# Optimization experiments

Hardware: AMD Instinct MI355X
Metric: run time of the kernel (lower is better)

The kernel has to match this reference:

```python
import jax, jax.numpy as jnp
import numpy as np

N = 100000
E = 1600000
D_IN = 128
D_OUT = 128
EPS_GIN = 0.0  # GIN epsilon from __init__
LN_EPS = 1e-5
PROJ_EPS = 1e-9


def setup_inputs() -> dict:
    key = jax.random.key(0)
    ks = jax.random.split(key, 9)
    x = jax.random.normal(ks[0], (N, D_IN), dtype=jnp.float32)
    edge_index = jax.random.randint(ks[1], (2, E), 0, N, dtype=jnp.int64)
    edge_weight = jax.random.normal(ks[2], (E,), dtype=jnp.float32)
    # MLP params (Linear(in,out) -> ReLU -> Linear(out,out)), torch default-ish init
    s1 = 1.0 / np.sqrt(D_IN)
    s2 = 1.0 / np.sqrt(D_OUT)
    W1 = jax.random.uniform(ks[3], (D_IN, D_OUT), jnp.float32, -s1, s1)
    b1 = jax.random.uniform(ks[4], (D_OUT,), jnp.float32, -s1, s1)
    W2 = jax.random.uniform(ks[5], (D_OUT, D_OUT), jnp.float32, -s2, s2)
    b2 = jax.random.uniform(ks[6], (D_OUT,), jnp.float32, -s2, s2)
    gamma = jnp.ones((D_OUT,), jnp.float32)
    beta = jnp.zeros((D_OUT,), jnp.float32)
    return {"x": x, "edge_index": edge_index, "edge_weight": edge_weight,
            "W1": W1, "b1": b1, "W2": W2, "b2": b2, "gamma": gamma, "beta": beta}


def _aggregate(x, edge_index, edge_weight):
    # Per-target-node softmax over edge weights, then weighted projective average.
    src = edge_index[0]
    tgt = edge_index[1]
    n = x.shape[0]
    m = jax.ops.segment_max(edge_weight, tgt, num_segments=n)          # [N]
    ew = jnp.exp(edge_weight - m[tgt])                                  # [E], stable softmax numerator
    denom = jax.ops.segment_sum(ew, tgt, num_segments=n)               # [N]
    w = ew / denom[tgt]                                                 # [E], per-node softmax weights
    msg = w[:, None] * x[src]                                           # [E, D]
    agg = jax.ops.segment_sum(msg, tgt, num_segments=n)                # [N, D] weighted sum
    # projective_average: normalize the weighted combination to the unit sphere
    norm = jnp.linalg.norm(agg, axis=-1, keepdims=True)
    return agg / (norm + PROJ_EPS)                                      # zero rows stay zero


def _layer_norm(h, gamma, beta):
    mu = jnp.mean(h, axis=-1, keepdims=True)
    var = jnp.var(h, axis=-1, keepdims=True)
    return gamma * (h - mu) * jax.lax.rsqrt(var + LN_EPS) + beta


def reference(x, edge_index, edge_weight, W1, b1, W2, b2, gamma, beta):
    neigh = _aggregate(x, edge_index, edge_weight)
    combined = (1.0 + EPS_GIN) * x + neigh
    h = jnp.maximum(combined @ W1 + b1, 0.0)
    h = h @ W2 + b2
    h = _layer_norm(h, gamma, beta)
    # dropout: eval mode -> identity
    return h
```

## Files before the change

### kernel.cpp

```cpp
#include <hip/hip_runtime.h>
#include <hip/hip_bf16.h>

#define D 128
#define CH 2048
#define BSH 9
#define SLAB 9216

typedef __attribute__((ext_vector_type(8))) short short8;
typedef __attribute__((ext_vector_type(4))) float f32x4;
typedef __attribute__((ext_vector_type(4))) int int4v;
typedef __attribute__((ext_vector_type(2))) int int2v;
typedef __attribute__((ext_vector_type(4))) float float4v;
typedef __attribute__((ext_vector_type(2))) float float2v;
typedef __attribute__((ext_vector_type(4))) unsigned uint4v;
typedef __attribute__((ext_vector_type(2))) unsigned uint2v;
typedef _Float16 half2_t __attribute__((ext_vector_type(2)));

__device__ __forceinline__ unsigned short us_bf16(float f) {
    return __bfloat16_as_ushort(__float2bfloat16(f));
}
__device__ __forceinline__ unsigned pack_bf16(float a, float b) {
    return (unsigned)us_bf16(a) | ((unsigned)us_bf16(b) << 16);
}
__device__ __forceinline__ unsigned pack_f16(float a, float b) {
    unsigned short ua = __builtin_bit_cast(unsigned short, (_Float16)a);
    unsigned short ub = __builtin_bit_cast(unsigned short, (_Float16)b);
    return (unsigned)ua | ((unsigned)ub << 16);
}
__device__ __forceinline__ float f16_lo(int y) {
    return (float)__builtin_bit_cast(_Float16, (unsigned short)(y & 0xffff));
}
__device__ __forceinline__ half2_t as_h2(unsigned u) {
    return __builtin_bit_cast(half2_t, u);
}
__device__ __forceinline__ int2v nt_load2(const int2* p) {
    return __builtin_nontemporal_load(reinterpret_cast<const int2v*>(p));
}

__global__ __launch_bounds__(256) void k_prep(const float* __restrict__ x,
                                              unsigned* __restrict__ xh,
                                              unsigned* __restrict__ xq, int nf4,
                                              const float* __restrict__ W1,
                                              const float* __restrict__ W2,
                                              unsigned short* __restrict__ W1t,
                                              unsigned short* __restrict__ W2t) {
    int i0 = blockIdx.x * blockDim.x + threadIdx.x;
    int stride = gridDim.x * blockDim.x;
    const float4v* x4 = reinterpret_cast<const float4v*>(x);
    uint2v* xh2 = reinterpret_cast<uint2v*>(xh);
    for (int i = i0; i < nf4; i += stride) {
        float4v v = x4[i];
        uint2v o;
        o.x = pack_f16(v.x, v.y);
        o.y = pack_f16(v.z, v.w);
        xh2[i] = o;
        int p = __builtin_amdgcn_cvt_pk_fp8_f32(v.x, v.y, 0, false);
        p = __builtin_amdgcn_cvt_pk_fp8_f32(v.z, v.w, p, true);
        xq[i] = (unsigned)p;
    }
    if (i0 < 16384) {
        int k = i0 >> 7, nn = i0 & 127;
        W1t[nn * 128 + k] = us_bf16(W1[i0]);
        W2t[nn * 128 + k] = us_bf16(W2[i0]);
    }
}

__global__ __launch_bounds__(256) void k_binA(
    const int* __restrict__ src, const int* __restrict__ tgt,
    const float* __restrict__ ew, int* __restrict__ bcnt,
    int2* __restrict__ stage, int E, int nbuk)
{
    __shared__ int2 recs[CH];
    __shared__ unsigned short bslot[CH];
    __shared__ int sh[256];
    __shared__ int lbase[256];
    __shared__ int gofs[256];

    int tid = threadIdx.x;
    int c0 = blockIdx.x * CH;
    int chunkCnt = min(CH, E - c0);

    sh[tid] = 0;
    __syncthreads();

    int myb[8], mypos[8], mysrc[8]; unsigned myy[8];
    #pragma unroll
    for (int k = 0; k < 8; ++k) {
        int idx = k * 256 + tid;
        myb[k] = -1;
        if (idx < chunkCnt) {
            int e = c0 + idx;
            int t = __builtin_nontemporal_load(&tgt[e]);
            int b = t >> BSH;
            float expw = __expf(__builtin_nontemporal_load(&ew[e]));
            unsigned short h = __builtin_bit_cast(unsigned short, (_Float16)expw);
            myb[k] = b;
            myy[k] = ((unsigned)(t & ((1 << BSH) - 1)) << 16) | (unsigned)h;
            mysrc[k] = __builtin_nontemporal_load(&src[e]);
            mypos[k] = atomicAdd(&sh[b], 1);
        }
    }
    __syncthreads();
    int cnt_b = sh[tid];
    for (int off = 1; off < 256; off <<= 1) {
        int o = (tid >= off) ? sh[tid - off] : 0;
        __syncthreads();
        sh[tid] += o;
        __syncthreads();
    }
    int lb = sh[tid] - cnt_b;
    lbase[tid] = lb;
    if (cnt_b > 0 && tid < nbuk) {
        int gb = atomicAdd(&bcnt[tid], cnt_b) + tid * SLAB;
        gofs[tid] = gb - lb;
    }
    __syncthreads();
    #pragma unroll
    for (int k = 0; k < 8; ++k) {
        if (myb[k] >= 0) {
            int slot = lbase[myb[k]] + mypos[k];
            recs[slot] = make_int2(mysrc[k], (int)myy[k]);
            bslot[slot] = (unsigned short)myb[k];
        }
    }
    __syncthreads();
    for (int i = tid; i < chunkCnt; i += 256) {
        int b = bslot[i];
        stage[gofs[b] + i] = recs[i];
    }
}

__global__ __launch_bounds__(256) void k_binB(
    const int* __restrict__ bcnt, const int2* __restrict__ stage,
    int2* __restrict__ csr, int* __restrict__ rowptr, int n)
{
    __shared__ int lcnt[1 << BSH];
    __shared__ float ldenom[1 << BSH];
    __shared__ int sc[256];
    int b = blockIdx.x;
    int tid = threadIdx.x;
    int node0 = b << BSH;
    int nn = min(1 << BSH, n - node0);
    int s0 = b * SLAB;
    int s1 = s0 + bcnt[b];

    for (int j = tid; j < (1 << BSH); j += 256) { lcnt[j] = 0; ldenom[j] = 0.f; }
    __syncthreads();

    for (int i = s0 + tid; i < s1; i += 256) {
        int2v rec = nt_load2(&stage[i]);
        int tl = ((unsigned)rec.y) >> 16;
        _Float16 hw = __builtin_bit_cast(_Float16, (unsigned short)(rec.y & 0xffff));
        atomicAdd(&lcnt[tl], 1);
        atomicAdd(&ldenom[tl], (float)hw);
    }
    __syncthreads();

    for (int j = tid; j < (1 << BSH); j += 256) {
        float d = ldenom[j];
        ldenom[j] = (d > 0.f) ? (1.f / d) : 0.f;
    }
    int v0 = lcnt[2 * tid], v1 = lcnt[2 * tid + 1];
    int tsum = v0 + v1;
    sc[tid] = tsum;
    __syncthreads();
    for (int off = 1; off < 256; off <<= 1) {
        int o = (tid >= off) ? sc[tid - off] : 0;
        __syncthreads();
        sc[tid] += o;
        __syncthreads();
    }
    int excl = sc[tid] - tsum;
    int p0 = s0 + excl, p1 = s0 + excl + v0;
    if (2 * tid < nn)     rowptr[node0 + 2 * tid] = p0;
    if (2 * tid + 1 < nn) rowptr[node0 + 2 * tid + 1] = p1;
    __syncthreads();
    lcnt[2 * tid] = p0;
    lcnt[2 * tid + 1] = p1;
    __syncthreads();

    for (int i = s0 + tid; i < s1; i += 256) {
        int2v rec = nt_load2(&stage[i]);
        int tl = ((unsigned)rec.y) >> 16;
        _Float16 hw = __builtin_bit_cast(_Float16, (unsigned short)(rec.y & 0xffff));
        float wn = (float)hw * ldenom[tl];
        unsigned short wb = __builtin_bit_cast(unsigned short, (_Float16)wn);
        unsigned wp = (unsigned)wb | ((unsigned)wb << 16);
        int pos = atomicAdd(&lcnt[tl], 1);
        csr[pos] = make_int2(rec.x, (int)wp);
    }
}

__global__ __launch_bounds__(256) void k_agg(
    const int* __restrict__ rowptr, const int* __restrict__ bcnt,
    const int2* __restrict__ csr,
    const uint4v* __restrict__ xq4, const uint4v* __restrict__ xh4,
    uint4v* __restrict__ cmb4, int n)
{
    int w = threadIdx.x >> 6;
    int lane = threadIdx.x & 63;
    int node = blockIdx.x * 4 + w;
    if (node >= n) node = n - 1;

    int b = node >> BSH;
    int r0 = rowptr[node];
    int r1;
    if ((((node + 1) & ((1 << BSH) - 1)) == 0) || (node + 1 >= n))
        r1 = b * SLAB + bcnt[b];
    else
        r1 = rowptr[node + 1];
    int cnt = r1 - r0;

    int eg = lane >> 3;
    int dg = lane & 7;

    float a[16];
    #pragma unroll
    for (int j = 0; j < 16; ++j) a[j] = 0.f;

    int last = (cnt > 0) ? cnt - 1 : 0;
    for (int base = 0; base < cnt; base += 32) {
        #pragma unroll
        for (int i = 0; i < 4; ++i) {
            if (base + i * 8 >= cnt) break;
            int e = base + i * 8 + eg;
            bool valid = e < cnt;
            int2v cr = nt_load2(&csr[r0 + (valid ? e : last)]);
            float wn = valid ? f16_lo(cr.y) : 0.f;
            uint4v q = xq4[cr.x * 8 + dg];
            #pragma unroll
            for (int h = 0; h < 4; ++h) {
                int word = (int)((h == 0) ? q.x : (h == 1) ? q.y : (h == 2) ? q.z : q.w);
                float2v flo = __builtin_amdgcn_cvt_pk_f32_fp8(word, false);
                float2v fhi = __builtin_amdgcn_cvt_pk_f32_fp8(word, true);
                a[h * 4 + 0] = fmaf(wn, flo.x, a[h * 4 + 0]);
                a[h * 4 + 1] = fmaf(wn, flo.y, a[h * 4 + 1]);
                a[h * 4 + 2] = fmaf(wn, fhi.x, a[h * 4 + 2]);
                a[h * 4 + 3] = fmaf(wn, fhi.y, a[h * 4 + 3]);
            }
        }
    }

    #pragma unroll
    for (int m = 8; m <= 32; m <<= 1)
        #pragma unroll
        for (int j = 0; j < 16; ++j)
            a[j] += __shfl_xor(a[j], m);

    float ss = 0.f;
    #pragma unroll
    for (int j = 0; j < 16; ++j) ss = fmaf(a[j], a[j], ss);
    #pragma unroll
    for (int m = 1; m <= 4; m <<= 1) ss += __shfl_xor(ss, m);
    float rn = 1.f / (sqrtf(ss) + 1e-9f);

    if (eg == 0) {
        #pragma unroll
        for (int h = 0; h < 2; ++h) {
            uint4v hx = xh4[node * 16 + dg * 2 + h];
            half2_t x0 = as_h2(hx.x), x1 = as_h2(hx.y), x2 = as_h2(hx.z), x3 = as_h2(hx.w);
            const float* ah = &a[h * 8];
            uint4v o;
            o.x = pack_bf16((float)x0.x + ah[0] * rn, (float)x0.y + ah[1] * rn);
            o.y = pack_bf16((float)x1.x + ah[2] * rn, (float)x1.y + ah[3] * rn);
            o.z = pack_bf16((float)x2.x + ah[4] * rn, (float)x2.y + ah[5] * rn);
            o.w = pack_bf16((float)x3.x + ah[6] * rn, (float)x3.y + ah[7] * rn);
            cmb4[node * 16 + dg * 2 + h] = o;
        }
    }
}

__global__ __launch_bounds__(256) void k_mlp(
    const uint4v* __restrict__ cmb4,
    const unsigned short* __restrict__ W1t, const unsigned short* __restrict__ W2t,
    const float* __restrict__ b1, const float* __restrict__ b2,
    const float* __restrict__ gamma, const float* __restrict__ beta,
    float* __restrict__ out, int n)
{
    __shared__ __align__(16) unsigned short sA[64][136];

    int node0 = blockIdx.x * 64;
    int w = threadIdx.x >> 6;
    int lane = threadIdx.x & 63;
    int lr = lane & 15;
    int lg = lane >> 4;
    int mr = w * 16;

    for (int idx = threadIdx.x; idx < 64 * 16; idx += 256) {
        int row = idx >> 4, seg = idx & 15;
        int gr = node0 + row; if (gr >= n) gr = n - 1;
        uint4v v = cmb4[gr * 16 + seg];
        *reinterpret_cast<uint4v*>(&sA[row][seg * 8]) = v;
    }
    __syncthreads();

    short8 aF[4];
    #pragma unroll
    for (int kt = 0; kt < 4; ++kt)
        aF[kt] = *reinterpret_cast<const short8*>(&sA[mr + lr][kt * 32 + lg * 8]);

    #pragma unroll
    for (int nt = 0; nt < 8; ++nt) {
        f32x4 c = {0.f, 0.f, 0.f, 0.f};
        #pragma unroll
        for (int kt = 0; kt < 4; ++kt) {
            short8 bF = *reinterpret_cast<const short8*>(
                &W1t[(nt * 16 + lr) * 128 + kt * 32 + lg * 8]);
            c = __builtin_amdgcn_mfma_f32_16x16x32_bf16(aF[kt], bF, c, 0, 0, 0);
        }
        float b1v = b1[nt * 16 + lr];
        #pragma unroll
        for (int reg = 0; reg < 4; ++reg) {
            float h = fmaxf(c[reg] + b1v, 0.f);
            sA[mr + lg * 4 + reg][nt * 16 + lr] = us_bf16(h);
        }
    }
    __syncthreads();

    short8 a2F[4];
    #pragma unroll
    for (int kt = 0; kt < 4; ++kt)
        a2F[kt] = *reinterpret_cast<const short8*>(&sA[mr + lr][kt * 32 + lg * 8]);

    f32x4 c2[8];
    float b2v[8], gv[8], bev[8];
    #pragma unroll
    for (int nt = 0; nt < 8; ++nt) {
        c2[nt] = (f32x4){0.f, 0.f, 0.f, 0.f};
        #pragma unroll
        for (int kt = 0; kt < 4; ++kt) {
            short8 bF = *reinterpret_cast<const short8*>(
                &W2t[(nt * 16 + lr) * 128 + kt * 32 + lg * 8]);
            c2[nt] = __builtin_amdgcn_mfma_f32_16x16x32_bf16(a2F[kt], bF, c2[nt], 0, 0, 0);
        }
        int col = nt * 16 + lr;
        b2v[nt] = b2[col]; gv[nt] = gamma[col]; bev[nt] = beta[col];
    }

    float rs[4] = {0.f, 0.f, 0.f, 0.f}, sq[4] = {0.f, 0.f, 0.f, 0.f};
    #pragma unroll
    for (int nt = 0; nt < 8; ++nt)
        #pragma unroll
        for (int reg = 0; reg < 4; ++reg) {
            float v = c2[nt][reg] + b2v[nt];
            rs[reg] += v; sq[reg] += v * v;
        }
    #pragma unroll
    for (int off = 1; off <= 8; off <<= 1)
        #pragma unroll
        for (int reg = 0; reg < 4; ++reg) {
            rs[reg] += __shfl_xor(rs[reg], off);
            sq[reg] += __shfl_xor(sq[reg], off);
        }
    float mu[4], rstd[4];
    #pragma unroll
    for (int reg = 0; reg < 4; ++reg) {
        mu[reg] = rs[reg] * (1.f / 128.f);
        float var = sq[reg] * (1.f / 128.f) - mu[reg] * mu[reg];
        rstd[reg] = rsqrtf(var + 1e-5f);
    }

    #pragma unroll
    for (int nt = 0; nt < 8; ++nt)
        #pragma unroll
        for (int reg = 0; reg < 4; ++reg) {
            int gr = node0 + mr + lg * 4 + reg;
            if (gr < n) {
                float v = c2[nt][reg] + b2v[nt];
                out[gr * 128 + nt * 16 + lr] = gv[nt] * (v - mu[reg]) * rstd[reg] + bev[nt];
            }
        }
}

extern "C" void kernel_launch(void* const* d_in, const int* in_sizes, int n_in,
                              void* d_out, int out_size, void* d_ws, size_t ws_size,
                              hipStream_t stream) {
    const float* x     = (const float*)d_in[0];
    const int*   ei    = (const int*)d_in[1];
    const float* ew    = (const float*)d_in[2];
    const float* W1    = (const float*)d_in[3];
    const float* b1    = (const float*)d_in[4];
    const float* W2    = (const float*)d_in[5];
    const float* b2    = (const float*)d_in[6];
    const float* gamma = (const float*)d_in[7];
    const float* beta  = (const float*)d_in[8];

    int n = in_sizes[0] / D;
    int E = in_sizes[2];
    const int* src = ei;
    const int* tgt = ei + E;

    int nbuk = (n + (1 << BSH) - 1) >> BSH;

    char* ws = (char*)d_ws;
    int2*     csr    = (int2*)ws;     ws += (size_t)nbuk * SLAB * sizeof(int2);
    unsigned* xh     = (unsigned*)ws; ws += (size_t)n * 64 * sizeof(unsigned);
    unsigned* xq     = (unsigned*)ws; ws += (size_t)n * 32 * sizeof(unsigned);
    unsigned* cmb    = (unsigned*)ws; ws += (size_t)n * 64 * sizeof(unsigned);
    unsigned short* W1t = (unsigned short*)ws; ws += 128 * 128 * sizeof(unsigned short);
    unsigned short* W2t = (unsigned short*)ws; ws += 128 * 128 * sizeof(unsigned short);
    int*      rowptr = (int*)ws;      ws += ((size_t)n + 1) * sizeof(int);
    int*      bcnt   = (int*)ws;      ws += 256 * sizeof(int);
    int2*     stage  = (int2*)cmb;

    hipMemsetAsync((void*)bcnt, 0, 256 * sizeof(int), stream);

    int nf4 = n * D / 4;
    k_prep<<<2048, 256, 0, stream>>>(x, xh, xq, nf4, W1, W2, W1t, W2t);

    int nchunk = (E + CH - 1) / CH;
    k_binA<<<nchunk, 256, 0, stream>>>(src, tgt, ew, bcnt, stage, E, nbuk);
    k_binB<<<nbuk, 256, 0, stream>>>(bcnt, stage, csr, rowptr, n);

    k_agg<<<(n + 3) / 4, 256, 0, stream>>>(rowptr, bcnt, csr,
                                           (const uint4v*)xq, (const uint4v*)xh,
                                           (uint4v*)cmb, n);

    k_mlp<<<(n + 63) / 64, 256, 0, stream>>>((const uint4v*)cmb, W1t, W2t,
                                             b1, b2, gamma, beta,
                                             (float*)d_out, n);
}
```

Before: 211.2 us.

## Drop softmax denominator, fuse prep into binning, use packed fp16 shuffle reduction

The softmax denominator pass in k_binB is removed and the raw exp weights go straight into the CSR. This relies on the projective normalisation dividing out any positive per-node scale, and it drops one LDS float-atomic pass plus a reciprocal step. The x/W conversion kernel is folded into the binning kernel as extra specialised blocks, saving a launch and letting the two run concurrently. The cross-lane reduction in k_agg now shuffles packed fp16 pairs scaled by 1/256, which halves the shuffle count at some precision and overflow risk.

```diff
diff --git a/kernel.cpp b/kernel.cpp
--- a/kernel.cpp
+++ b/kernel.cpp
@@ -5,6 +5,7 @@
 #define CH 2048
 #define BSH 9
 #define SLAB 9216
+#define PREP_BLK 1024
 
 typedef __attribute__((ext_vector_type(8))) short short8;
 typedef __attribute__((ext_vector_type(4))) float f32x4;
@@ -37,38 +38,14 @@
     return __builtin_nontemporal_load(reinterpret_cast<const int2v*>(p));
 }
 
-__global__ __launch_bounds__(256) void k_prep(const float* __restrict__ x,
-                                              unsigned* __restrict__ xh,
-                                              unsigned* __restrict__ xq, int nf4,
-                                              const float* __restrict__ W1,
-                                              const float* __restrict__ W2,
-                                              unsigned short* __restrict__ W1t,
-                                              unsigned short* __restrict__ W2t) {
-    int i0 = blockIdx.x * blockDim.x + threadIdx.x;
-    int stride = gridDim.x * blockDim.x;
-    const float4v* x4 = reinterpret_cast<const float4v*>(x);
-    uint2v* xh2 = reinterpret_cast<uint2v*>(xh);
-    for (int i = i0; i < nf4; i += stride) {
-        float4v v = x4[i];
-        uint2v o;
-        o.x = pack_f16(v.x, v.y);
-        o.y = pack_f16(v.z, v.w);
-        xh2[i] = o;
-        int p = __builtin_amdgcn_cvt_pk_fp8_f32(v.x, v.y, 0, false);
-        p = __builtin_amdgcn_cvt_pk_fp8_f32(v.z, v.w, p, true);
-        xq[i] = (unsigned)p;
-    }
-    if (i0 < 16384) {
-        int k = i0 >> 7, nn = i0 & 127;
-        W1t[nn * 128 + k] = us_bf16(W1[i0]);
-        W2t[nn * 128 + k] = us_bf16(W2[i0]);
-    }
-}
-
-__global__ __launch_bounds__(256) void k_binA(
+__global__ __launch_bounds__(256) void k_prepbinA(
     const int* __restrict__ src, const int* __restrict__ tgt,
     const float* __restrict__ ew, int* __restrict__ bcnt,
-    int2* __restrict__ stage, int E, int nbuk)
+    int2* __restrict__ stage, int E, int nbuk, int nchunk,
+    const float* __restrict__ x, unsigned* __restrict__ xh,
+    unsigned* __restrict__ xq, int nf4,
+    const float* __restrict__ W1, const float* __restrict__ W2,
+    unsigned short* __restrict__ W1t, unsigned short* __restrict__ W2t)
 {
     __shared__ int2 recs[CH];
     __shared__ unsigned short bslot[CH];
@@ -77,6 +54,31 @@
     __shared__ int gofs[256];
 
     int tid = threadIdx.x;
+
+    if (blockIdx.x >= (unsigned)nchunk) {
+        int pb = blockIdx.x - nchunk;
+        int i0 = pb * 256 + tid;
+        int stride = PREP_BLK * 256;
+        const float4v* x4 = reinterpret_cast<const float4v*>(x);
+        uint2v* xh2 = reinterpret_cast<uint2v*>(xh);
+        for (int i = i0; i < nf4; i += stride) {
+            float4v v = x4[i];
+            uint2v o;
+            o.x = pack_f16(v.x, v.y);
+            o.y = pack_f16(v.z, v.w);
+            xh2[i] = o;
+            int p = __builtin_amdgcn_cvt_pk_fp8_f32(v.x, v.y, 0, false);
+            p = __builtin_amdgcn_cvt_pk_fp8_f32(v.z, v.w, p, true);
+            xq[i] = (unsigned)p;
+        }
+        if (i0 < 16384) {
+            int k = i0 >> 7, nn = i0 & 127;
+            W1t[nn * 128 + k] = us_bf16(W1[i0]);
+            W2t[nn * 128 + k] = us_bf16(W2[i0]);
+        }
+        return;
+    }
+
     int c0 = blockIdx.x * CH;
     int chunkCnt = min(CH, E - c0);
 
@@ -135,7 +137,6 @@
     int2* __restrict__ csr, int* __restrict__ rowptr, int n)
 {
     __shared__ int lcnt[1 << BSH];
-    __shared__ float ldenom[1 << BSH];
     __shared__ int sc[256];
     int b = blockIdx.x;
     int tid = threadIdx.x;
@@ -144,22 +145,15 @@
     int s0 = b * SLAB;
     int s1 = s0 + bcnt[b];
 
-    for (int j = tid; j < (1 << BSH); j += 256) { lcnt[j] = 0; ldenom[j] = 0.f; }
+    for (int j = tid; j < (1 << BSH); j += 256) lcnt[j] = 0;
     __syncthreads();
 
     for (int i = s0 + tid; i < s1; i += 256) {
         int2v rec = nt_load2(&stage[i]);
-        int tl = ((unsigned)rec.y) >> 16;
-        _Float16 hw = __builtin_bit_cast(_Float16, (unsigned short)(rec.y & 0xffff));
-        atomicAdd(&lcnt[tl], 1);
-        atomicAdd(&ldenom[tl], (float)hw);
-    }
-    __syncthreads();
-
-    for (int j = tid; j < (1 << BSH); j += 256) {
-        float d = ldenom[j];
-        ldenom[j] = (d > 0.f) ? (1.f / d) : 0.f;
-    }
+        atomicAdd(&lcnt[((unsigned)rec.y) >> 16], 1);
+    }
+    __syncthreads();
+
     int v0 = lcnt[2 * tid], v1 = lcnt[2 * tid + 1];
     int tsum = v0 + v1;
     sc[tid] = tsum;
@@ -181,13 +175,8 @@
 
     for (int i = s0 + tid; i < s1; i += 256) {
         int2v rec = nt_load2(&stage[i]);
-        int tl = ((unsigned)rec.y) >> 16;
-        _Float16 hw = __builtin_bit_cast(_Float16, (unsigned short)(rec.y & 0xffff));
-        float wn = (float)hw * ldenom[tl];
-        unsigned short wb = __builtin_bit_cast(unsigned short, (_Float16)wn);
-        unsigned wp = (unsigned)wb | ((unsigned)wb << 16);
-        int pos = atomicAdd(&lcnt[tl], 1);
-        csr[pos] = make_int2(rec.x, (int)wp);
+        int pos = atomicAdd(&lcnt[((unsigned)rec.y) >> 16], 1);
+        csr[pos] = make_int2(rec.x, rec.y);
     }
 }
 
@@ -242,14 +231,30 @@
     }
 
     #pragma unroll
+    for (int j = 0; j < 16; ++j) a[j] *= 0.00390625f;
+    unsigned u[8];
+    #pragma unroll
+    for (int j = 0; j < 8; ++j)
+        u[j] = __builtin_bit_cast(unsigned,
+                   __builtin_amdgcn_cvt_pkrtz(a[2 * j], a[2 * j + 1]));
+    #pragma unroll
     for (int m = 8; m <= 32; m <<= 1)
         #pragma unroll
-        for (int j = 0; j < 16; ++j)
-            a[j] += __shfl_xor(a[j], m);
+        for (int j = 0; j < 8; ++j) {
+            half2_t s = as_h2(u[j]) + as_h2((unsigned)__shfl_xor((int)u[j], m));
+            u[j] = __builtin_bit_cast(unsigned, s);
+        }
+    float af[16];
+    #pragma unroll
+    for (int j = 0; j < 8; ++j) {
+        half2_t s = as_h2(u[j]);
+        af[2 * j] = (float)s.x;
+        af[2 * j + 1] = (float)s.y;
+    }
 
     float ss = 0.f;
     #pragma unroll
-    for (int j = 0; j < 16; ++j) ss = fmaf(a[j], a[j], ss);
+    for (int j = 0; j < 16; ++j) ss = fmaf(af[j], af[j], ss);
     #pragma unroll
     for (int m = 1; m <= 4; m <<= 1) ss += __shfl_xor(ss, m);
     float rn = 1.f / (sqrtf(ss) + 1e-9f);
@@ -259,7 +264,7 @@
         for (int h = 0; h < 2; ++h) {
             uint4v hx = xh4[node * 16 + dg * 2 + h];
             half2_t x0 = as_h2(hx.x), x1 = as_h2(hx.y), x2 = as_h2(hx.z), x3 = as_h2(hx.w);
-            const float* ah = &a[h * 8];
+            const float* ah = &af[h * 8];
             uint4v o;
             o.x = pack_bf16((float)x0.x + ah[0] * rn, (float)x0.y + ah[1] * rn);
             o.y = pack_bf16((float)x1.x + ah[2] * rn, (float)x1.y + ah[3] * rn);
@@ -406,10 +411,11 @@
     hipMemsetAsync((void*)bcnt, 0, 256 * sizeof(int), stream);
 
     int nf4 = n * D / 4;
-    k_prep<<<2048, 256, 0, stream>>>(x, xh, xq, nf4, W1, W2, W1t, W2t);
-
     int nchunk = (E + CH - 1) / CH;
-    k_binA<<<nchunk, 256, 0, stream>>>(src, tgt, ew, bcnt, stage, E, nbuk);
+    k_prepbinA<<<nchunk + PREP_BLK, 256, 0, stream>>>(
+        src, tgt, ew, bcnt, stage, E, nbuk, nchunk,
+        x, xh, xq, nf4, W1, W2, W1t, W2t);
+
     k_binB<<<nbuk, 256, 0, stream>>>(bcnt, stage, csr, rowptr, n);
 
     k_agg<<<(n + 3) / 4, 256, 0, stream>>>(rowptr, bcnt, csr,
```

New measurement: 202.0 us (median of 2 runs). 1.05x faster.
